# Optimization experiments

Hardware: AMD Instinct MI355X
Metric: run time of the kernel (lower is better)

Reference implementation:

```python
import jax, jax.numpy as jnp
import numpy as np

N_NODES = 100000
N_EDGES = 1600000
F = 64
UNITS = 64


def setup_inputs() -> dict:
    key = jax.random.key(0)
    k = jax.random.split(key, 8)
    x = jax.random.normal(k[0], (N_NODES, F), dtype=jnp.float32)
    edge_index = jax.random.randint(k[1], (2, N_EDGES), 0, N_NODES, dtype=jnp.int32)
    edge_weight = jnp.ones((N_EDGES,), dtype=jnp.float32)
    # glorot-uniform-ish params
    def glorot(kk, shape):
        lim = np.sqrt(6.0 / (shape[0] + shape[1]))
        return jax.random.uniform(kk, shape, dtype=jnp.float32, minval=-lim, maxval=lim)
    mlp_kernel = glorot(k[2], (F, UNITS))
    mlp_bias = jnp.zeros((UNITS,), dtype=jnp.float32)
    neighs_kernel = glorot(k[3], (UNITS, UNITS))
    self_kernel = glorot(k[4], (F, UNITS))
    bias = jnp.zeros((2 * UNITS,), dtype=jnp.float32)
    return {"x": x, "edge_index": edge_index, "edge_weight": edge_weight,
            "mlp_kernel": mlp_kernel, "mlp_bias": mlp_bias,
            "neighs_kernel": neighs_kernel, "self_kernel": self_kernel, "bias": bias}


def reference(x, edge_index, edge_weight, mlp_kernel, mlp_bias, neighs_kernel, self_kernel, bias):
    num_nodes = x.shape[0]
    row, col = edge_index[0], edge_index[1]
    # gcn_mapper: neighbor message scaled by edge weight (original forces weights to 1)
    neighbor_x = x[col] * edge_weight[:, None]            # [E, F]
    h = jax.nn.relu(neighbor_x @ mlp_kernel + mlp_bias)   # [E, U]
    # unsorted_segment_mean over destination row (empty segments -> 0, matching TF)
    seg_sum = jax.ops.segment_sum(h, row, num_segments=num_nodes)              # [N, U]
    cnt = jax.ops.segment_sum(jnp.ones_like(row, dtype=h.dtype), row, num_segments=num_nodes)
    reduced_h = seg_sum / jnp.maximum(cnt, 1.0)[:, None]
    from_neighs = reduced_h @ neighs_kernel               # [N, U]
    from_x = x @ self_kernel                              # [N, U]
    out = jnp.concatenate([from_neighs, from_x], axis=1) + bias
    out = jax.nn.relu(out)                                # [N, 2U]
    return out
```

## Files before the change

### kernel.cpp

```cpp
#include <hip/hip_runtime.h>

#define MAXSLICE 12544
#define NBH 32

static __device__ __forceinline__ float relu_f(float v) { return fmaxf(v, 0.f); }

static __device__ __forceinline__ unsigned short f2bf(float f) {
  unsigned u = __float_as_uint(f);
  u += 0x7fffu + ((u >> 16) & 1u);
  return (unsigned short)(u >> 16);
}
static __device__ __forceinline__ float bf2f(unsigned short h) {
  return __uint_as_float(((unsigned)h) << 16);
}

__global__ __launch_bounds__(256) void k_node_dual_gemm(
    const float* __restrict__ x, const float* __restrict__ mk,
    const float* __restrict__ sk, const float* __restrict__ bias,
    unsigned short* __restrict__ xwh, float* __restrict__ out, int n_nodes)
{
  __shared__ float s_mk[64][64];
  __shared__ float s_sk[64][64];
  __shared__ float s_xT[64][68];
  const int tid = threadIdx.x;
  for (int i = tid; i < 4096; i += 256) {
    s_mk[i >> 6][i & 63] = mk[i];
    s_sk[i >> 6][i & 63] = sk[i];
  }
  const int node0 = blockIdx.x * 64;
  for (int i = tid; i < 4096; i += 256) {
    int nl = i >> 6, f = i & 63;
    int n = node0 + nl;
    s_xT[f][nl] = (n < n_nodes) ? x[(size_t)n * 64 + f] : 0.f;
  }
  __syncthreads();
  const int g  = tid >> 4;
  const int ub = (tid & 15) * 4;
  float am[4][4] = {{0.f}};
  float as[4][4] = {{0.f}};
  for (int f = 0; f < 64; ++f) {
    float4 wm = *(const float4*)&s_mk[f][ub];
    float4 ws = *(const float4*)&s_sk[f][ub];
    float4 xv = *(const float4*)&s_xT[f][4 * g];
    const float xs[4] = {xv.x, xv.y, xv.z, xv.w};
#pragma unroll
    for (int j = 0; j < 4; ++j) {
      am[j][0] += xs[j] * wm.x; am[j][1] += xs[j] * wm.y;
      am[j][2] += xs[j] * wm.z; am[j][3] += xs[j] * wm.w;
      as[j][0] += xs[j] * ws.x; as[j][1] += xs[j] * ws.y;
      as[j][2] += xs[j] * ws.z; as[j][3] += xs[j] * ws.w;
    }
  }
  float4 bv = *(const float4*)&bias[64 + ub];
#pragma unroll
  for (int j = 0; j < 4; ++j) {
    int n = node0 + 4 * g + j;
    if (n >= n_nodes) break;
    ushort4 o1 = make_ushort4(f2bf(am[j][0]), f2bf(am[j][1]),
                              f2bf(am[j][2]), f2bf(am[j][3]));
    *(ushort4*)&xwh[(size_t)n * 64 + ub] = o1;
    *(float4*)&out[(size_t)n * 128 + 64 + ub] =
        make_float4(relu_f(as[j][0] + bv.x), relu_f(as[j][1] + bv.y),
                    relu_f(as[j][2] + bv.z), relu_f(as[j][3] + bv.w));
  }
}

__global__ __launch_bounds__(256) void k_count(
    const int* __restrict__ row, int* __restrict__ cnt, int n_edges)
{
  int e = blockIdx.x * 256 + threadIdx.x;
  if (e < n_edges) atomicAdd(&cnt[row[e]], 1);
}

__global__ __launch_bounds__(256) void k_build_sliced(
    const int* __restrict__ row, const int* __restrict__ col,
    const float* __restrict__ ew, int* __restrict__ off,
    int2* __restrict__ elist, int n_edges, int n_nodes)
{
  const int slice = blockIdx.x & 7;
  const int vb    = blockIdx.x >> 3;
  const int nvb   = gridDim.x >> 3;
  const int sliceN = (n_nodes + 7) >> 3;
  const int lo = slice * sliceN;
  const int hi = min(lo + sliceN, n_nodes);
  for (int e = vb * 256 + threadIdx.x; e < n_edges; e += nvb * 256) {
    int r = row[e];
    if (r >= lo && r < hi) {
      int pos = atomicAdd(&off[r], 1);
      elist[pos] = make_int2(col[e], __float_as_int(ew[e]));
    }
  }
}

__global__ __launch_bounds__(1024) void k_bsum(
    const int* __restrict__ cnt, int* __restrict__ bsum, int n)
{
  __shared__ int s[1024];
  int tid = threadIdx.x;
  int i = blockIdx.x * 1024 + tid;
  s[tid] = (i < n) ? cnt[i] : 0;
  __syncthreads();
  for (int d = 512; d > 0; d >>= 1) {
    if (tid < d) s[tid] += s[tid + d];
    __syncthreads();
  }
  if (tid == 0) bsum[blockIdx.x] = s[0];
}

__global__ __launch_bounds__(1024) void k_boffs(
    const int* __restrict__ cnt, const int* __restrict__ bsum,
    int* __restrict__ off, int n, int nb)
{
  __shared__ int s[1024];
  __shared__ int sp[128];
  int tid = threadIdx.x;
  if (tid < 128) {
    int acc = 0;
    for (int j = tid; j < blockIdx.x && j < nb; j += 128) acc += bsum[j];
    sp[tid] = acc;
  }
  int i = blockIdx.x * 1024 + tid;
  int v = (i < n) ? cnt[i] : 0;
  s[tid] = v;
  __syncthreads();
  for (int d = 64; d > 0; d >>= 1) {
    if (tid < d) sp[tid] += sp[tid + d];
    __syncthreads();
  }
  for (int d = 1; d < 1024; d <<= 1) {
    int t = (tid >= d) ? s[tid - d] : 0;
    __syncthreads();
    s[tid] += t;
    __syncthreads();
  }
  if (i < n) off[i] = s[tid] - v + sp[0];
}

__global__ __launch_bounds__(256) void k_bin(
    const int* __restrict__ row, const int* __restrict__ col,
    const float* __restrict__ ew,
    int* __restrict__ brow, int* __restrict__ bcol, float* __restrict__ bew,
    int* __restrict__ bcur, int n_edges, int sliceN, int cap)
{
  __shared__ int s_wcnt[4][8];
  __shared__ int s_base[8];
  const int tid  = threadIdx.x;
  const int wave = tid >> 6;
  const int lane = tid & 63;
  const unsigned usliceN = (unsigned)sliceN;
  const int stride = gridDim.x * 1024;
  for (int e0 = blockIdx.x * 1024; e0 < n_edges; e0 += stride) {
    const int e = e0 + 4 * tid;
    int   rr[4], cc[4];
    float ww[4];
    int   ss[4];
    if (e + 3 < n_edges) {
      int4 r4   = *(const int4*)&row[e];
      int4 c4   = *(const int4*)&col[e];
      float4 w4 = *(const float4*)&ew[e];
      rr[0] = r4.x; rr[1] = r4.y; rr[2] = r4.z; rr[3] = r4.w;
      cc[0] = c4.x; cc[1] = c4.y; cc[2] = c4.z; cc[3] = c4.w;
      ww[0] = w4.x; ww[1] = w4.y; ww[2] = w4.z; ww[3] = w4.w;
#pragma unroll
      for (int j = 0; j < 4; ++j) ss[j] = (int)((unsigned)rr[j] / usliceN);
    } else {
#pragma unroll
      for (int j = 0; j < 4; ++j) {
        int ej = e + j;
        bool v = ej < n_edges;
        rr[j] = v ? row[ej] : 0;
        cc[j] = v ? col[ej] : 0;
        ww[j] = v ? ew[ej]  : 0.f;
        ss[j] = v ? (int)((unsigned)rr[j] / usliceN) : -1;
      }
    }
#pragma unroll
    for (int b = 0; b < 8; ++b) {
      int c = 0;
#pragma unroll
      for (int j = 0; j < 4; ++j) c += __popcll(__ballot(ss[j] == b));
      if (lane == 0) s_wcnt[wave][b] = c;
    }
    __syncthreads();
    if (wave == 0 && lane < 8) {
      const int b = lane;
      int t0 = s_wcnt[0][b], t1 = s_wcnt[1][b], t2 = s_wcnt[2][b], t3 = s_wcnt[3][b];
      int tot = t0 + t1 + t2 + t3;
      int base = tot ? atomicAdd(&bcur[b], tot) : 0;
      s_base[b] = base;
      s_wcnt[0][b] = 0;
      s_wcnt[1][b] = t0;
      s_wcnt[2][b] = t0 + t1;
      s_wcnt[3][b] = t0 + t1 + t2;
    }
    __syncthreads();
#pragma unroll
    for (int b = 0; b < 8; ++b) {
      const int wbase = s_base[b] + s_wcnt[wave][b];
      int off_local = 0;
#pragma unroll
      for (int j = 0; j < 4; ++j) {
        unsigned long long mm = __ballot(ss[j] == b);
        if (ss[j] == b) {
          int rank = __popcll(mm & ((1ull << lane) - 1ull));
          int p = b * cap + wbase + off_local + rank;
          if (p < (b + 1) * cap) {
            brow[p] = rr[j];
            bcol[p] = cc[j];
            bew[p]  = ww[j];
          }
        }
        off_local += __popcll(mm);
      }
    }
    __syncthreads();
  }
}

__global__ __launch_bounds__(256) void k_hist(
    const int* __restrict__ brow, const int* __restrict__ bcur,
    int* __restrict__ hist, int cap, int chunk, int sliceN)
{
  __shared__ int h[MAXSLICE];
  const int s   = blockIdx.x & 7;
  const int blk = blockIdx.x >> 3;
  const int tid = threadIdx.x;
  for (int i = tid; i < MAXSLICE; i += 256) h[i] = 0;
  __syncthreads();
  const int n_s  = min(bcur[s], cap);
  const int lo_e = blk * chunk;
  const int hi_e = min(lo_e + chunk, n_s);
  const int base = s * cap;
  const int lo   = s * sliceN;
  for (int i = lo_e + tid; i < hi_e; i += 256) {
    atomicAdd(&h[brow[base + i] - lo], 1);
  }
  __syncthreads();
  int* hrow = hist + (size_t)(s * NBH + blk) * MAXSLICE;
  for (int i = tid; i < MAXSLICE / 4; i += 256) {
    ((int4*)hrow)[i] = ((const int4*)h)[i];
  }
}

__global__ __launch_bounds__(256) void k_colscan(
    int* __restrict__ hist, int* __restrict__ cnt, int sliceN, int n_nodes)
{
  const int s  = blockIdx.x & 7;
  const int cb = blockIdx.x >> 3;
  const int b0 = cb * 1024 + threadIdx.x * 4;
  if (b0 >= sliceN) return;
  int4 acc = make_int4(0, 0, 0, 0);
  int* hs = hist + (size_t)s * NBH * MAXSLICE;
#pragma unroll 4
  for (int blk = 0; blk < NBH; ++blk) {
    int4* p = (int4*)(hs + (size_t)blk * MAXSLICE + b0);
    int4 v = *p;
    *p = acc;
    acc.x += v.x; acc.y += v.y; acc.z += v.z; acc.w += v.w;
  }
  const int node = s * sliceN + b0;
  if (b0 + 3 < sliceN && node + 3 < n_nodes) {
    *(int4*)&cnt[node] = acc;
  } else {
    int a[4] = {acc.x, acc.y, acc.z, acc.w};
    for (int j = 0; j < 4; ++j)
      if (b0 + j < sliceN && node + j < n_nodes) cnt[node + j] = a[j];
  }
}

__global__ __launch_bounds__(256) void k_place(
    const int* __restrict__ brow, const int* __restrict__ bcol,
    const float* __restrict__ bew, const int* __restrict__ bcur,
    const int* __restrict__ hist, const int* __restrict__ off,
    int2* __restrict__ elist, int cap, int chunk, int sliceN, int n_nodes)
{
  __shared__ int cur[MAXSLICE];
  const int s   = blockIdx.x & 7;
  const int blk = blockIdx.x >> 3;
  const int tid = threadIdx.x;
  const int lo  = s * sliceN;
  const int hi  = min(lo + sliceN, n_nodes);
  const int nb  = hi - lo;
  const int* hrow = hist + (size_t)(s * NBH + blk) * MAXSLICE;
  for (int i = tid; i < nb; i += 256) cur[i] = off[lo + i] + hrow[i];
  __syncthreads();
  const int n_s  = min(bcur[s], cap);
  const int lo_e = blk * chunk;
  const int hi_e = min(lo_e + chunk, n_s);
  const int base = s * cap;
  for (int i = lo_e + tid; i < hi_e; i += 256) {
    int r = brow[base + i] - lo;
    int p = atomicAdd(&cur[r], 1);
    elist[p] = make_int2(bcol[base + i], __float_as_int(bew[base + i]));
  }
}

__global__ __launch_bounds__(256) void k_scatter(
    const int* __restrict__ brow, const int* __restrict__ bcol,
    const float* __restrict__ bew, const int* __restrict__ bcur,
    int* __restrict__ off, int2* __restrict__ elist, int cap)
{
  const int s   = blockIdx.x & 7;
  const int vb  = blockIdx.x >> 3;
  const int nvb = gridDim.x >> 3;
  const int n   = min(bcur[s], cap);
  const int base = s * cap;
  for (int i = vb * 256 + threadIdx.x; i < n; i += nvb * 256) {
    int r = brow[base + i];
    int pos = atomicAdd(&off[r], 1);
    elist[pos] = make_int2(bcol[base + i], __float_as_int(bew[base + i]));
  }
}

__global__ __launch_bounds__(256) void k_fused_reduce_gemm(
    const int* __restrict__ cnt, const int* __restrict__ off,
    const int2* __restrict__ elist, const unsigned short* __restrict__ xwh,
    const float* __restrict__ mb, const float* __restrict__ nk,
    const float* __restrict__ bias, float* __restrict__ out, int n_nodes,
    int starts)
{
  __shared__ float s_nk[64][64];
  __shared__ float s_rh[16][68];
  const int tid = threadIdx.x;
  for (int i = tid; i < 1024; i += 256) {
    *(float4*)&s_nk[0][4 * i] = *(const float4*)&nk[4 * i];
  }
  const int node_l = tid >> 4;
  const int q = tid & 15;
  const int n = blockIdx.x * 16 + node_l;
  float4 acc = make_float4(0.f, 0.f, 0.f, 0.f);
  if (n < n_nodes) {
    const float4 mbq = *(const float4*)&mb[4 * q];
    const int c = cnt[n];
    int i = off[n] - (starts ? 0 : c);
    const int end = i + c;
    for (; i + 2 <= end; i += 2) {
      int2 e0 = elist[i];
      int2 e1 = elist[i + 1];
      ushort4 u0 = *(const ushort4*)&xwh[(size_t)e0.x * 64 + 4 * q];
      ushort4 u1 = *(const ushort4*)&xwh[(size_t)e1.x * 64 + 4 * q];
      float w0 = __int_as_float(e0.y);
      float w1 = __int_as_float(e1.y);
      acc.x += relu_f(w0 * bf2f(u0.x) + mbq.x);
      acc.y += relu_f(w0 * bf2f(u0.y) + mbq.y);
      acc.z += relu_f(w0 * bf2f(u0.z) + mbq.z);
      acc.w += relu_f(w0 * bf2f(u0.w) + mbq.w);
      acc.x += relu_f(w1 * bf2f(u1.x) + mbq.x);
      acc.y += relu_f(w1 * bf2f(u1.y) + mbq.y);
      acc.z += relu_f(w1 * bf2f(u1.z) + mbq.z);
      acc.w += relu_f(w1 * bf2f(u1.w) + mbq.w);
    }
    if (i < end) {
      int2 e0 = elist[i];
      ushort4 u0 = *(const ushort4*)&xwh[(size_t)e0.x * 64 + 4 * q];
      float w0 = __int_as_float(e0.y);
      acc.x += relu_f(w0 * bf2f(u0.x) + mbq.x);
      acc.y += relu_f(w0 * bf2f(u0.y) + mbq.y);
      acc.z += relu_f(w0 * bf2f(u0.z) + mbq.z);
      acc.w += relu_f(w0 * bf2f(u0.w) + mbq.w);
    }
    const float inv = 1.0f / fmaxf((float)c, 1.0f);
    acc.x *= inv; acc.y *= inv; acc.z *= inv; acc.w *= inv;
  }
  *(float4*)&s_rh[node_l][4 * q] = acc;
  __syncthreads();
  float4 o = make_float4(0.f, 0.f, 0.f, 0.f);
  for (int f = 0; f < 64; ++f) {
    float rv = s_rh[node_l][f];
    float4 wv = *(const float4*)&s_nk[f][4 * q];
    o.x += rv * wv.x; o.y += rv * wv.y; o.z += rv * wv.z; o.w += rv * wv.w;
  }
  if (n < n_nodes) {
    float4 bv = *(const float4*)&bias[4 * q];
    *(float4*)&out[(size_t)n * 128 + 4 * q] =
        make_float4(relu_f(o.x + bv.x), relu_f(o.y + bv.y),
                    relu_f(o.z + bv.z), relu_f(o.w + bv.w));
  }
}

extern "C" void kernel_launch(void* const* d_in, const int* in_sizes, int n_in,
                              void* d_out, int out_size, void* d_ws, size_t ws_size,
                              hipStream_t stream) {
  const float* x    = (const float*)d_in[0];
  const int*   ei   = (const int*)d_in[1];
  const float* ew   = (const float*)d_in[2];
  const float* mk   = (const float*)d_in[3];
  const float* mb   = (const float*)d_in[4];
  const float* nk   = (const float*)d_in[5];
  const float* sk   = (const float*)d_in[6];
  const float* bias = (const float*)d_in[7];
  float* out = (float*)d_out;

  const int n_nodes = in_sizes[0] / 64;
  const int n_edges = in_sizes[2];
  const int* row = ei;
  const int* col = ei + n_edges;

  unsigned short* xwh = (unsigned short*)d_ws;
  int*  cnt  = (int*)(xwh + (size_t)n_nodes * 64);
  int*  bcur = cnt + n_nodes;
  int*  off  = bcur + 8;
  int*  bsum = off + n_nodes;
  size_t ebytes = ((size_t)((char*)(bsum + 128) - (char*)d_ws) + 7) & ~(size_t)7;
  int2* elist = (int2*)((char*)d_ws + ebytes);
  const int cap = (n_edges >> 3) + 8192;
  int*   brow = (int*)(elist + n_edges);
  int*   bcol = brow + (size_t)8 * cap;
  float* bew  = (float*)(bcol + (size_t)8 * cap);
  size_t need_b = (size_t)((char*)(bew + (size_t)8 * cap) - (char*)d_ws);
  size_t hoff = (need_b + 15) & ~(size_t)15;
  int*   hist = (int*)((char*)d_ws + hoff);
  size_t need_a = hoff + (size_t)8 * NBH * MAXSLICE * sizeof(int);

  const int nb_scan = (n_nodes + 1023) / 1024;
  const int sliceN = (n_nodes + 7) >> 3;
  const int nbn = (n_nodes + 63) / 64;
  const int nbf = (n_nodes + 15) / 16;
  const int chunk = (cap + NBH - 1) / NBH;

  if (ws_size >= need_a && sliceN <= MAXSLICE) {
    hipMemsetAsync(bcur, 0, 8 * sizeof(int), stream);
    k_node_dual_gemm<<<nbn, 256, 0, stream>>>(x, mk, sk, bias, xwh, out, n_nodes);
    int nbb = (n_edges + 1023) / 1024;
    if (nbb > 1024) nbb = 1024;
    k_bin<<<nbb, 256, 0, stream>>>(row, col, ew, brow, bcol, bew, bcur,
                                   n_edges, sliceN, cap);
    k_hist<<<8 * NBH, 256, 0, stream>>>(brow, bcur, hist, cap, chunk, sliceN);
    const int ncb = (sliceN + 1023) / 1024;
    k_colscan<<<8 * ncb, 256, 0, stream>>>(hist, cnt, sliceN, n_nodes);
    k_bsum<<<nb_scan, 1024, 0, stream>>>(cnt, bsum, n_nodes);
    k_boffs<<<nb_scan, 1024, 0, stream>>>(cnt, bsum, off, n_nodes, nb_scan);
    k_place<<<8 * NBH, 256, 0, stream>>>(brow, bcol, bew, bcur, hist, off,
                                         elist, cap, chunk, sliceN, n_nodes);
    k_fused_reduce_gemm<<<nbf, 256, 0, stream>>>(cnt, off, elist, xwh, mb, nk,
                                                 bias, out, n_nodes, 1);
  } else if (ws_size >= need_b) {
    hipMemsetAsync(cnt, 0, (size_t)(n_nodes + 8) * sizeof(int), stream);
    k_node_dual_gemm<<<nbn, 256, 0, stream>>>(x, mk, sk, bias, xwh, out, n_nodes);
    int nbb = (n_edges + 1023) / 1024;
    if (nbb > 1024) nbb = 1024;
    k_bin<<<nbb, 256, 0, stream>>>(row, col, ew, brow, bcol, bew, bcur,
                                   n_edges, sliceN, cap);
    const int nbe = (n_edges + 255) / 256;
    k_count<<<nbe, 256, 0, stream>>>(row, cnt, n_edges);
    k_bsum<<<nb_scan, 1024, 0, stream>>>(cnt, bsum, n_nodes);
    k_boffs<<<nb_scan, 1024, 0, stream>>>(cnt, bsum, off, n_nodes, nb_scan);
    k_scatter<<<1024, 256, 0, stream>>>(brow, bcol, bew, bcur, off, elist, cap);
    k_fused_reduce_gemm<<<nbf, 256, 0, stream>>>(cnt, off, elist, xwh, mb, nk,
                                                 bias, out, n_nodes, 0);
  } else {
    hipMemsetAsync(cnt, 0, (size_t)n_nodes * sizeof(int), stream);
    k_node_dual_gemm<<<nbn, 256, 0, stream>>>(x, mk, sk, bias, xwh, out, n_nodes);
    const int nbe = (n_edges + 255) / 256;
    k_count<<<nbe, 256, 0, stream>>>(row, cnt, n_edges);
    k_bsum<<<nb_scan, 1024, 0, stream>>>(cnt, bsum, n_nodes);
    k_boffs<<<nb_scan, 1024, 0, stream>>>(cnt, bsum, off, n_nodes, nb_scan);
    k_build_sliced<<<1024, 256, 0, stream>>>(row, col, ew, off, elist,
                                             n_edges, n_nodes);
    k_fused_reduce_gemm<<<nbf, 256, 0, stream>>>(cnt, off, elist, xwh, mb, nk,
                                                 bias, out, n_nodes, 0);
  }
}
```

Before: 272.7 us.

## Stage binned edges in LDS, pack col/weight pairs, unroll gather loop by 8

The binning kernel now stages each 1024-edge tile in shared memory, ordered by bin, then writes it out with contiguous per-bin runs instead of scattered per-lane stores. Column and weight are packed into one int2 array, so the later place and scatter kernels copy one 8-byte value instead of assembling two loads. The neighbour-gather loop in the fused reduce kernel is unrolled to 8 edges with all loads issued first, to raise memory-level parallelism. The bin grid cap is also raised. The cost is 12 KB of extra LDS and one more barrier per tile in the binning kernel, plus higher register use in the reduce kernel.

```diff
diff --git a/kernel.cpp b/kernel.cpp
--- a/kernel.cpp
+++ b/kernel.cpp
@@ -139,11 +139,15 @@
 __global__ __launch_bounds__(256) void k_bin(
     const int* __restrict__ row, const int* __restrict__ col,
     const float* __restrict__ ew,
-    int* __restrict__ brow, int* __restrict__ bcol, float* __restrict__ bew,
+    int* __restrict__ brow, int2* __restrict__ bpair,
     int* __restrict__ bcur, int n_edges, int sliceN, int cap)
 {
-  __shared__ int s_wcnt[4][8];
-  __shared__ int s_base[8];
+  __shared__ int  s_wcnt[4][8];
+  __shared__ int  s_tot[8];
+  __shared__ int  s_toff[8];
+  __shared__ int  s_gaddr[8];
+  __shared__ int  s_rowst[1024];
+  __shared__ int2 s_pairst[1024];
   const int tid  = threadIdx.x;
   const int wave = tid >> 6;
   const int lane = tid & 63;
@@ -186,31 +190,45 @@
       const int b = lane;
       int t0 = s_wcnt[0][b], t1 = s_wcnt[1][b], t2 = s_wcnt[2][b], t3 = s_wcnt[3][b];
       int tot = t0 + t1 + t2 + t3;
-      int base = tot ? atomicAdd(&bcur[b], tot) : 0;
-      s_base[b] = base;
+      s_tot[b] = tot;
       s_wcnt[0][b] = 0;
       s_wcnt[1][b] = t0;
       s_wcnt[2][b] = t0 + t1;
       s_wcnt[3][b] = t0 + t1 + t2;
+      int gbase = tot ? atomicAdd(&bcur[b], tot) : 0;
+      int pre = 0;
+#pragma unroll
+      for (int j2 = 0; j2 < 8; ++j2) pre += (j2 < b) ? s_tot[j2] : 0;
+      s_toff[b]  = pre;
+      s_gaddr[b] = b * cap + gbase - pre;
     }
     __syncthreads();
 #pragma unroll
     for (int b = 0; b < 8; ++b) {
-      const int wbase = s_base[b] + s_wcnt[wave][b];
+      const int sb = s_toff[b] + s_wcnt[wave][b];
       int off_local = 0;
 #pragma unroll
       for (int j = 0; j < 4; ++j) {
         unsigned long long mm = __ballot(ss[j] == b);
         if (ss[j] == b) {
           int rank = __popcll(mm & ((1ull << lane) - 1ull));
-          int p = b * cap + wbase + off_local + rank;
-          if (p < (b + 1) * cap) {
-            brow[p] = rr[j];
-            bcol[p] = cc[j];
-            bew[p]  = ww[j];
-          }
+          int slot = sb + off_local + rank;
+          s_rowst[slot]  = rr[j];
+          s_pairst[slot] = make_int2(cc[j], __float_as_int(ww[j]));
         }
         off_local += __popcll(mm);
+      }
+    }
+    __syncthreads();
+    const int total = s_toff[7] + s_tot[7];
+    for (int i2 = tid; i2 < total; i2 += 256) {
+      int b = 0;
+#pragma unroll
+      for (int j2 = 1; j2 < 8; ++j2) b += (i2 >= s_toff[j2]) ? 1 : 0;
+      int a = s_gaddr[b] + i2;
+      if (a < (b + 1) * cap) {
+        brow[a]  = s_rowst[i2];
+        bpair[a] = s_pairst[i2];
       }
     }
     __syncthreads();
@@ -269,10 +287,10 @@
 }
 
 __global__ __launch_bounds__(256) void k_place(
-    const int* __restrict__ brow, const int* __restrict__ bcol,
-    const float* __restrict__ bew, const int* __restrict__ bcur,
-    const int* __restrict__ hist, const int* __restrict__ off,
-    int2* __restrict__ elist, int cap, int chunk, int sliceN, int n_nodes)
+    const int* __restrict__ brow, const int2* __restrict__ bpair,
+    const int* __restrict__ bcur, const int* __restrict__ hist,
+    const int* __restrict__ off, int2* __restrict__ elist,
+    int cap, int chunk, int sliceN, int n_nodes)
 {
   __shared__ int cur[MAXSLICE];
   const int s   = blockIdx.x & 7;
@@ -291,14 +309,14 @@
   for (int i = lo_e + tid; i < hi_e; i += 256) {
     int r = brow[base + i] - lo;
     int p = atomicAdd(&cur[r], 1);
-    elist[p] = make_int2(bcol[base + i], __float_as_int(bew[base + i]));
+    elist[p] = bpair[base + i];
   }
 }
 
 __global__ __launch_bounds__(256) void k_scatter(
-    const int* __restrict__ brow, const int* __restrict__ bcol,
-    const float* __restrict__ bew, const int* __restrict__ bcur,
-    int* __restrict__ off, int2* __restrict__ elist, int cap)
+    const int* __restrict__ brow, const int2* __restrict__ bpair,
+    const int* __restrict__ bcur, int* __restrict__ off,
+    int2* __restrict__ elist, int cap)
 {
   const int s   = blockIdx.x & 7;
   const int vb  = blockIdx.x >> 3;
@@ -308,7 +326,7 @@
   for (int i = vb * 256 + threadIdx.x; i < n; i += nvb * 256) {
     int r = brow[base + i];
     int pos = atomicAdd(&off[r], 1);
-    elist[pos] = make_int2(bcol[base + i], __float_as_int(bew[base + i]));
+    elist[pos] = bpair[base + i];
   }
 }
 
@@ -334,23 +352,42 @@
     const int c = cnt[n];
     int i = off[n] - (starts ? 0 : c);
     const int end = i + c;
-    for (; i + 2 <= end; i += 2) {
-      int2 e0 = elist[i];
-      int2 e1 = elist[i + 1];
-      ushort4 u0 = *(const ushort4*)&xwh[(size_t)e0.x * 64 + 4 * q];
-      ushort4 u1 = *(const ushort4*)&xwh[(size_t)e1.x * 64 + 4 * q];
-      float w0 = __int_as_float(e0.y);
-      float w1 = __int_as_float(e1.y);
-      acc.x += relu_f(w0 * bf2f(u0.x) + mbq.x);
-      acc.y += relu_f(w0 * bf2f(u0.y) + mbq.y);
-      acc.z += relu_f(w0 * bf2f(u0.z) + mbq.z);
-      acc.w += relu_f(w0 * bf2f(u0.w) + mbq.w);
-      acc.x += relu_f(w1 * bf2f(u1.x) + mbq.x);
-      acc.y += relu_f(w1 * bf2f(u1.y) + mbq.y);
-      acc.z += relu_f(w1 * bf2f(u1.z) + mbq.z);
-      acc.w += relu_f(w1 * bf2f(u1.w) + mbq.w);
-    }
-    if (i < end) {
+    for (; i + 8 <= end; i += 8) {
+      int2 e[8];
+#pragma unroll
+      for (int j = 0; j < 8; ++j) e[j] = elist[i + j];
+      ushort4 u[8];
+#pragma unroll
+      for (int j = 0; j < 8; ++j)
+        u[j] = *(const ushort4*)&xwh[(size_t)e[j].x * 64 + 4 * q];
+#pragma unroll
+      for (int j = 0; j < 8; ++j) {
+        float w = __int_as_float(e[j].y);
+        acc.x += relu_f(w * bf2f(u[j].x) + mbq.x);
+        acc.y += relu_f(w * bf2f(u[j].y) + mbq.y);
+        acc.z += relu_f(w * bf2f(u[j].z) + mbq.z);
+        acc.w += relu_f(w * bf2f(u[j].w) + mbq.w);
+      }
+    }
+    if (i + 4 <= end) {
+      int2 e[4];
+#pragma unroll
+      for (int j = 0; j < 4; ++j) e[j] = elist[i + j];
+      ushort4 u[4];
+#pragma unroll
+      for (int j = 0; j < 4; ++j)
+        u[j] = *(const ushort4*)&xwh[(size_t)e[j].x * 64 + 4 * q];
+#pragma unroll
+      for (int j = 0; j < 4; ++j) {
+        float w = __int_as_float(e[j].y);
+        acc.x += relu_f(w * bf2f(u[j].x) + mbq.x);
+        acc.y += relu_f(w * bf2f(u[j].y) + mbq.y);
+        acc.z += relu_f(w * bf2f(u[j].z) + mbq.z);
+        acc.w += relu_f(w * bf2f(u[j].w) + mbq.w);
+      }
+      i += 4;
+    }
+    for (; i < end; ++i) {
       int2 e0 = elist[i];
       ushort4 u0 = *(const ushort4*)&xwh[(size_t)e0.x * 64 + 4 * q];
       float w0 = __int_as_float(e0.y);
@@ -404,12 +441,12 @@
   size_t ebytes = ((size_t)((char*)(bsum + 128) - (char*)d_ws) + 7) & ~(size_t)7;
   int2* elist = (int2*)((char*)d_ws + ebytes);
   const int cap = (n_edges >> 3) + 8192;
-  int*   brow = (int*)(elist + n_edges);
-  int*   bcol = brow + (size_t)8 * cap;
-  float* bew  = (float*)(bcol + (size_t)8 * cap);
-  size_t need_b = (size_t)((char*)(bew + (size_t)8 * cap) - (char*)d_ws);
+  int*  brow  = (int*)(elist + n_edges);
+  size_t pboff = (((size_t)((char*)(brow + (size_t)8 * cap) - (char*)d_ws)) + 7) & ~(size_t)7;
+  int2* bpair = (int2*)((char*)d_ws + pboff);
+  size_t need_b = (size_t)((char*)(bpair + (size_t)8 * cap) - (char*)d_ws);
   size_t hoff = (need_b + 15) & ~(size_t)15;
-  int*   hist = (int*)((char*)d_ws + hoff);
+  int*  hist  = (int*)((char*)d_ws + hoff);
   size_t need_a = hoff + (size_t)8 * NBH * MAXSLICE * sizeof(int);
 
   const int nb_scan = (n_nodes + 1023) / 1024;
@@ -422,15 +459,15 @@
     hipMemsetAsync(bcur, 0, 8 * sizeof(int), stream);
     k_node_dual_gemm<<<nbn, 256, 0, stream>>>(x, mk, sk, bias, xwh, out, n_nodes);
     int nbb = (n_edges + 1023) / 1024;
-    if (nbb > 1024) nbb = 1024;
-    k_bin<<<nbb, 256, 0, stream>>>(row, col, ew, brow, bcol, bew, bcur,
+    if (nbb > 2048) nbb = 2048;
+    k_bin<<<nbb, 256, 0, stream>>>(row, col, ew, brow, bpair, bcur,
                                    n_edges, sliceN, cap);
     k_hist<<<8 * NBH, 256, 0, stream>>>(brow, bcur, hist, cap, chunk, sliceN);
     const int ncb = (sliceN + 1023) / 1024;
     k_colscan<<<8 * ncb, 256, 0, stream>>>(hist, cnt, sliceN, n_nodes);
     k_bsum<<<nb_scan, 1024, 0, stream>>>(cnt, bsum, n_nodes);
     k_boffs<<<nb_scan, 1024, 0, stream>>>(cnt, bsum, off, n_nodes, nb_scan);
-    k_place<<<8 * NBH, 256, 0, stream>>>(brow, bcol, bew, bcur, hist, off,
+    k_place<<<8 * NBH, 256, 0, stream>>>(brow, bpair, bcur, hist, off,
                                          elist, cap, chunk, sliceN, n_nodes);
     k_fused_reduce_gemm<<<nbf, 256, 0, stream>>>(cnt, off, elist, xwh, mb, nk,
                                                  bias, out, n_nodes, 1);
@@ -438,14 +475,14 @@
     hipMemsetAsync(cnt, 0, (size_t)(n_nodes + 8) * sizeof(int), stream);
     k_node_dual_gemm<<<nbn, 256, 0, stream>>>(x, mk, sk, bias, xwh, out, n_nodes);
     int nbb = (n_edges + 1023) / 1024;
-    if (nbb > 1024) nbb = 1024;
-    k_bin<<<nbb, 256, 0, stream>>>(row, col, ew, brow, bcol, bew, bcur,
+    if (nbb > 2048) nbb = 2048;
+    k_bin<<<nbb, 256, 0, stream>>>(row, col, ew, brow, bpair, bcur,
                                    n_edges, sliceN, cap);
     const int nbe = (n_edges + 255) / 256;
     k_count<<<nbe, 256, 0, stream>>>(row, cnt, n_edges);
     k_bsum<<<nb_scan, 1024, 0, stream>>>(cnt, bsum, n_nodes);
     k_boffs<<<nb_scan, 1024, 0, stream>>>(cnt, bsum, off, n_nodes, nb_scan);
-    k_scatter<<<1024, 256, 0, stream>>>(brow, bcol, bew, bcur, off, elist, cap);
+    k_scatter<<<1024, 256, 0, stream>>>(brow, bpair, bcur, off, elist, cap);
     k_fused_reduce_gemm<<<nbf, 256, 0, stream>>>(cnt, off, elist, xwh, mb, nk,
                                                  bias, out, n_nodes, 0);
   } else {
```

Result: faster. 256.8 us (-5.9%).
